# Kernel tuning notes

Hardware: AMD Instinct MI355X
Metric: run time of the kernel (lower is better)

Reference implementation:

```python
import jax, jax.numpy as jnp
import numpy as np

N = 100   # num_nodes
D = 32    # num_dags
B = 8192  # batch_size
H = 32    # MLP hidden width


def setup_inputs() -> dict:
    key = jax.random.key(0)
    ks = jax.random.split(key, 6)
    x = jax.random.normal(ks[0], (B, N), dtype=jnp.float32)
    # binary adjacency masks for each sampled DAG
    A = (jax.random.uniform(ks[1], (D, N, N)) < 0.5).astype(jnp.float32)
    # per-dag topological order: a permutation of the N nodes
    order = jax.vmap(lambda k: jax.random.permutation(k, N))(
        jax.random.split(ks[2], D)).astype(jnp.int32)
    do_idx = 0  # intervened node
    # per-node MLP params: Linear(N+1, H) -> LeakyReLU -> Linear(H, 1)
    W1 = jax.random.normal(ks[3], (N, H, N + 1), dtype=jnp.float32) * (1.0 / np.sqrt(N + 1))
    b1 = jnp.zeros((N, H), dtype=jnp.float32)
    W2 = jax.random.normal(ks[4], (N, H), dtype=jnp.float32) * (1.0 / np.sqrt(H))
    b2 = jnp.zeros((N,), dtype=jnp.float32)
    return {"x": x, "A": A, "order": order, "do_idx": do_idx,
            "W1": W1, "b1": b1, "W2": W2, "b2": b2}


def reference(x, A, order, do_idx, W1, b1, W2, b2):
    Bn, Nn = x.shape
    # intervention: zero incoming edges of do_idx
    A = A.at[:, :, do_idx].set(0.0)

    def run_dag(A_d, order_d):
        def step(outputs, node):
            mask = A_d[:, node]                      # [N] parents of `node`
            ins = jnp.concatenate(
                [outputs * mask[None, :], x[:, node][:, None]], axis=1)  # [B, N+1]
            h = jax.nn.leaky_relu(ins @ W1[node].T + b1[node])           # [B, H]
            out = h @ W2[node] + b2[node]                                # [B]
            val = jnp.where(node == do_idx, x[:, node], out)
            return outputs.at[:, node].set(val), None

        outs, _ = jax.lax.scan(step, jnp.zeros((Bn, Nn), x.dtype), order_d)
        return outs  # [B, N]

    return jax.vmap(run_dag)(A, order)  # [D, B, N]
```

## Files before the change

### kernel.cpp

```cpp
#include <hip/hip_runtime.h>
#include <hip/hip_fp16.h>

#define NN 100
#define HH 32
#define BB 8192
#define DD 32
#define KP 128
#define TPB 512

typedef _Float16 f16x8 __attribute__((ext_vector_type(8)));
typedef _Float16 f16x2 __attribute__((ext_vector_type(2)));
typedef __fp16 fph2 __attribute__((ext_vector_type(2)));
typedef float f32x4 __attribute__((ext_vector_type(4)));
typedef unsigned short ushort_t;
typedef unsigned int uint_t;
union FU { uint4 u; f16x8 h; };
union PU { fph2 p; f16x2 h; uint_t u; };

#define AS_GLOBAL __attribute__((address_space(1)))
#define AS_LDS    __attribute__((address_space(3)))

__global__ void prep_xt(const float* __restrict__ x, float* __restrict__ xT) {
  int idx = blockIdx.x * 256 + threadIdx.x;
  if (idx >= BB * NN) return;
  int b = idx & (BB - 1);
  int n = idx >> 13;
  xT[idx] = x[(size_t)b * NN + n];
}

__global__ void prep_w1m(const float* __restrict__ A, const float* __restrict__ W1,
                         const float* __restrict__ b1, ushort_t* __restrict__ W1M) {
  int idx = blockIdx.x * 256 + threadIdx.x;
  int tile = idx >> 12;
  int d = tile / NN;
  int node = tile - d * NN;
  int rem = idx & 4095;
  int j = rem >> 7;
  int k = rem & 127;
  float v = 0.f;
  if (k < NN) {
    float m = A[((size_t)d * NN + k) * NN + node];
    v = (m != 0.f) ? W1[((size_t)node * HH + j) * (NN + 1) + k] : 0.f;
  } else if (k == NN) {
    v = W1[((size_t)node * HH + j) * (NN + 1) + NN];
  } else if (k == NN + 1) {
    v = b1[node * HH + j];
  }
  int t = (j * KP + k) ^ ((j & 7) << 3);
  W1M[(size_t)tile * 4096 + t] = __half_as_ushort(__float2half_rn(v));
}

__global__ void prep_epi3(const float* __restrict__ W2, const float* __restrict__ b2,
                          uint_t* __restrict__ epi) {
  int idx = blockIdx.x * 256 + threadIdx.x;
  if (idx >= NN * 20) return;
  int node = idx / 20;
  int c = idx - node * 20;
  uint_t v = 0u;
  if (c < 16) {
    uint_t lo = __half_as_ushort(__float2half_rn(W2[node * HH + 2 * c]));
    uint_t hi = __half_as_ushort(__float2half_rn(W2[node * HH + 2 * c + 1]));
    v = lo | (hi << 16);
  } else if (c == 16) {
    v = __float_as_uint(b2[node]);
  }
  epi[idx] = v;
}

#define EPI_OFF 65536
#define SMEM_BYTES (65536 + 8000)

__global__ __launch_bounds__(TPB, 4) void dag_mfma_ss(
    const float* __restrict__ xT,
    const int* __restrict__ order,
    const int* __restrict__ do_idx_p,
    const ushort_t* __restrict__ W1M,
    const uint_t* __restrict__ epi_g,
    float* __restrict__ out)
{
  __shared__ __align__(16) char smem[SMEM_BYTES];
  ushort_t* stage = (ushort_t*)smem;
  const char* sp = (const char*)smem;
  uint_t* epi_l = (uint_t*)(smem + EPI_OFF);

  const int d = blockIdx.y;
  const int bx = blockIdx.x;
  const int tid = threadIdx.x;
  const int w = tid >> 6;
  const int lane = tid & 63;
  const int g = lane >> 4;
  const int n16 = lane & 15;
  const int di = __builtin_amdgcn_readfirstlane(do_idx_p[0]);
  const int rowbase = bx * 512 + w * 64 + n16;

  {
    const uint4* s4 = (const uint4*)epi_g;
    uint4* d4 = (uint4*)epi_l;
    for (int i = tid; i < 500; i += TPB) d4[i] = s4[i];
  }

  const ushort_t* Wd = W1M + (size_t)d * NN * 4096;
  const int* ord = order + d * NN;

  int vs[4];
#pragma unroll
  for (int S = 0; S < 4; ++S) {
    int hw = n16 * 128 + ((8 * g) ^ ((n16 & 3) << 3)) + 32 * (S ^ ((n16 >> 2) & 1));
    vs[S] = 2 * hw + 32768;
  }

  int nd[4], nn[4];
#pragma unroll
  for (int q = 0; q < 4; ++q) nd[q] = __builtin_amdgcn_readfirstlane(ord[q]);
#pragma unroll
  for (int q = 0; q < 4; ++q) {
    const ushort_t* gsrc = Wd + (size_t)nd[q] * 4096 + tid * 8;
    __builtin_amdgcn_global_load_lds((const AS_GLOBAL void*)gsrc,
        (AS_LDS void*)(stage + q * 4096 + (w << 9)), 16, 0, 0);
  }
  float xq[4][4];
#pragma unroll
  for (int q = 0; q < 4; ++q) {
    const float* xp = xT + (size_t)nd[q] * BB + rowbase;
#pragma unroll
    for (int nt = 0; nt < 4; ++nt) xq[q][nt] = xp[nt * 16];
  }

  uint4 breg[4][4];
#pragma unroll
  for (int nt = 0; nt < 4; ++nt) {
#pragma unroll
    for (int S = 0; S < 4; ++S) breg[nt][S] = make_uint4(0u, 0u, 0u, 0u);
    breg[nt][3].z = (g == 0) ? 0x3C000000u : 0u;
  }

  const f32x4 zero4 = {0.f, 0.f, 0.f, 0.f};
  PU c001; c001.u = 0x211F211Fu;

#pragma unroll 1
  for (int ss = 0; ss < 25; ++ss) {
    asm volatile("s_waitcnt vmcnt(0) lgkmcnt(0)" ::: "memory");
    __builtin_amdgcn_s_barrier();
    __builtin_amdgcn_sched_barrier(0);

#pragma unroll
    for (int S = 0; S < 4; ++S) vs[S] ^= 32768;

    const bool more = (ss < 24);
    if (more) {
#pragma unroll
      for (int q = 0; q < 4; ++q)
        nn[q] = __builtin_amdgcn_readfirstlane(ord[4 * (ss + 1) + q]);
      const int dsts = (((ss + 1) & 1) << 14);
#pragma unroll
      for (int q = 0; q < 4; ++q) {
        const ushort_t* gsrc = Wd + (size_t)nn[q] * 4096 + tid * 8;
        __builtin_amdgcn_global_load_lds((const AS_GLOBAL void*)gsrc,
            (AS_LDS void*)(stage + dsts + q * 4096 + (w << 9)), 16, 0, 0);
      }
    }

#pragma unroll
    for (int q = 0; q < 4; ++q) {
      const int node = nd[q];

#pragma unroll
      for (int nt = 0; nt < 4; ++nt) {
        uint_t old = breg[nt][3].z;
        uint_t ins = (old & 0xFFFF0000u) |
                     (uint_t)__half_as_ushort(__float2half_rn(xq[q][nt]));
        breg[nt][3].z = (g == 0) ? ins : old;
      }

      float val[4];
      if (node != di) {
        const char* ep = (const char*)epi_l + node * 80;
        const uint2 wlo = *(const uint2*)(ep + 8 * g);
        const uint2 whi = *(const uint2*)(ep + 32 + 8 * g);
        const float b2n = *(const float*)(ep + 64);

        f32x4 acc[4][2];
        __builtin_amdgcn_s_setprio(1);
#pragma unroll
        for (int S = 0; S < 4; ++S) {
          FU a0, a1;
          a0.u = *(const uint4*)(sp + vs[S] + q * 8192);
          a1.u = *(const uint4*)(sp + vs[S] + q * 8192 + 4096);
#pragma unroll
          for (int nt = 0; nt < 4; ++nt) {
            FU bu; bu.u = breg[nt][S];
            if (S == 0) {
              acc[nt][0] = __builtin_amdgcn_mfma_f32_16x16x32_f16(a0.h, bu.h, zero4, 0, 0, 0);
              acc[nt][1] = __builtin_amdgcn_mfma_f32_16x16x32_f16(a1.h, bu.h, zero4, 0, 0, 0);
            } else {
              acc[nt][0] = __builtin_amdgcn_mfma_f32_16x16x32_f16(a0.h, bu.h, acc[nt][0], 0, 0, 0);
              acc[nt][1] = __builtin_amdgcn_mfma_f32_16x16x32_f16(a1.h, bu.h, acc[nt][1], 0, 0, 0);
            }
          }
        }
        __builtin_amdgcn_s_setprio(0);

        PU w01, w23, w45, w67;
        w01.u = wlo.x; w23.u = wlo.y; w45.u = whi.x; w67.u = whi.y;
#pragma unroll
        for (int nt = 0; nt < 4; ++nt) {
#if __has_builtin(__builtin_amdgcn_fdot2)
          PU h01, h23, h45, h67;
          h01.p = __builtin_amdgcn_cvt_pkrtz(acc[nt][0][0], acc[nt][0][1]);
          h23.p = __builtin_amdgcn_cvt_pkrtz(acc[nt][0][2], acc[nt][0][3]);
          h45.p = __builtin_amdgcn_cvt_pkrtz(acc[nt][1][0], acc[nt][1][1]);
          h67.p = __builtin_amdgcn_cvt_pkrtz(acc[nt][1][2], acc[nt][1][3]);
          h01.p = __builtin_elementwise_max(h01.p, h01.p * c001.p);
          h23.p = __builtin_elementwise_max(h23.p, h23.p * c001.p);
          h45.p = __builtin_elementwise_max(h45.p, h45.p * c001.p);
          h67.p = __builtin_elementwise_max(h67.p, h67.p * c001.p);
          float p = __builtin_amdgcn_fdot2(h01.h, w01.h, 0.f, false);
          p = __builtin_amdgcn_fdot2(h23.h, w23.h, p, false);
          p = __builtin_amdgcn_fdot2(h45.h, w45.h, p, false);
          p = __builtin_amdgcn_fdot2(h67.h, w67.h, p, false);
#else
          float p = 0.f;
          const uint_t wu0[2] = {w01.u, w23.u};
          const uint_t wu1[2] = {w45.u, w67.u};
#pragma unroll
          for (int r4 = 0; r4 < 4; ++r4) {
            float wv0 = __half2float(__ushort_as_half(
                (ushort_t)((wu0[r4 >> 1] >> ((r4 & 1) * 16)) & 0xFFFFu)));
            float wv1 = __half2float(__ushort_as_half(
                (ushort_t)((wu1[r4 >> 1] >> ((r4 & 1) * 16)) & 0xFFFFu)));
            float h0 = acc[nt][0][r4]; h0 = fmaxf(h0, 0.01f * h0);
            float h1 = acc[nt][1][r4]; h1 = fmaxf(h1, 0.01f * h1);
            p = fmaf(wv0, h0, p);
            p = fmaf(wv1, h1, p);
          }
#endif
          p += __shfl_xor(p, 16, 64);
          p += __shfl_xor(p, 32, 64);
          val[nt] = p + b2n;
        }
      } else {
#pragma unroll
        for (int nt = 0; nt < 4; ++nt) val[nt] = xq[q][nt];
      }

      if (more) {
        const float* xp = xT + (size_t)nn[q] * BB + rowbase;
#pragma unroll
        for (int nt = 0; nt < 4; ++nt) xq[q][nt] = xp[nt * 16];
      }

      const int sn = node >> 5;
      const int en2 = (node >> 1) & 3;
      const int gn = (node >> 3) & 3;
      const int hin = node & 1;
      const bool own = (g == gn);
      ushort_t hv[4];
#pragma unroll
      for (int nt = 0; nt < 4; ++nt) hv[nt] = __half_as_ushort(__float2half_rn(val[nt]));
#pragma unroll
      for (int S = 0; S < 4; ++S) {
        if (S != sn) continue;
#pragma unroll
        for (int nt = 0; nt < 4; ++nt) {
          uint4& Bq = breg[nt][S];
          uint_t hvn = (uint_t)hv[nt];
          if (en2 == 0) {
            uint_t old = Bq.x;
            uint_t nw = hin ? ((old & 0x0000FFFFu) | (hvn << 16)) : ((old & 0xFFFF0000u) | hvn);
            Bq.x = own ? nw : old;
          } else if (en2 == 1) {
            uint_t old = Bq.y;
            uint_t nw = hin ? ((old & 0x0000FFFFu) | (hvn << 16)) : ((old & 0xFFFF0000u) | hvn);
            Bq.y = own ? nw : old;
          } else if (en2 == 2) {
            uint_t old = Bq.z;
            uint_t nw = hin ? ((old & 0x0000FFFFu) | (hvn << 16)) : ((old & 0xFFFF0000u) | hvn);
            Bq.z = own ? nw : old;
          } else {
            uint_t old = Bq.w;
            uint_t nw = hin ? ((old & 0x0000FFFFu) | (hvn << 16)) : ((old & 0xFFFF0000u) | hvn);
            Bq.w = own ? nw : old;
          }
        }
      }
    }

#pragma unroll
    for (int q = 0; q < 4; ++q) nd[q] = nn[q];
  }

  ushort_t* tbuf = (ushort_t*)smem;
  for (int c = 0; c < 8; ++c) {
    __syncthreads();
    if (w == c) {
#pragma unroll
      for (int nt = 0; nt < 4; ++nt) {
        int r = nt * 16 + n16;
#pragma unroll
        for (int S = 0; S < 4; ++S) {
          int k = 32 * S + 8 * g;
          *(uint2*)&tbuf[r * 132 + k] = make_uint2(breg[nt][S].x, breg[nt][S].y);
          *(uint2*)&tbuf[r * 132 + k + 4] = make_uint2(breg[nt][S].z, breg[nt][S].w);
        }
      }
    }
    __syncthreads();
    const size_t obase = ((size_t)d * BB + bx * 512 + c * 64) * NN;
    for (int idx = tid; idx < 64 * NN; idx += TPB) {
      int rl = idx / NN;
      int col = idx - rl * NN;
      out[obase + idx] = __half2float(__ushort_as_half(tbuf[rl * 132 + col]));
    }
  }
}

extern "C" void kernel_launch(void* const* d_in, const int* in_sizes, int n_in,
                              void* d_out, int out_size, void* d_ws, size_t ws_size,
                              hipStream_t stream) {
  const float* x     = (const float*)d_in[0];
  const float* A     = (const float*)d_in[1];
  const int* order   = (const int*)d_in[2];
  const int* do_idx  = (const int*)d_in[3];
  const float* W1    = (const float*)d_in[4];
  const float* b1    = (const float*)d_in[5];
  const float* W2    = (const float*)d_in[6];
  const float* b2    = (const float*)d_in[7];
  float* out = (float*)d_out;

  char* ws = (char*)d_ws;
  const size_t XT_B = 3276800UL;
  const size_t W1M_B = (size_t)DD * NN * 4096 * 2;
  float* xT     = (float*)ws;
  ushort_t* W1M = (ushort_t*)(ws + XT_B);
  uint_t* epi   = (uint_t*)(ws + XT_B + W1M_B);

  hipLaunchKernelGGL(prep_xt, dim3((BB * NN) / 256), dim3(256), 0, stream, x, xT);
  hipLaunchKernelGGL(prep_w1m, dim3((DD * NN * 4096) / 256), dim3(256), 0, stream,
                     A, W1, b1, W1M);
  hipLaunchKernelGGL(prep_epi3, dim3((NN * 20 + 255) / 256), dim3(256), 0, stream,
                     W2, b2, epi);
  hipLaunchKernelGGL(dag_mfma_ss, dim3(BB / 512, DD), dim3(TPB), 0, stream,
                     xT, order, do_idx, W1M, epi, out);
}
```

Measured before the change: 305.6 us.

## Stage fp16 x columns into LDS via async global_load_lds double buffer

The transposed x is now stored as fp16 in the prep kernel, which halves its footprint. The main kernel no longer issues per-thread global float loads into registers. Instead, one wave per node slot prefetches the next step's x column into a double-buffered LDS region with global_load_lds, alongside the W1 tiles. Each step then reads x from LDS, which frees about 16 VGPRs and takes global latency off the critical path. The cost is 8KB more LDS per block, which may affect occupancy, and the do_idx passthrough value is now rounded to fp16 before being written out.

```diff
diff --git a/kernel.cpp b/kernel.cpp
--- a/kernel.cpp
+++ b/kernel.cpp
@@ -20,12 +20,12 @@
 #define AS_GLOBAL __attribute__((address_space(1)))
 #define AS_LDS    __attribute__((address_space(3)))
 
-__global__ void prep_xt(const float* __restrict__ x, float* __restrict__ xT) {
+__global__ void prep_xth(const float* __restrict__ x, ushort_t* __restrict__ xTh) {
   int idx = blockIdx.x * 256 + threadIdx.x;
   if (idx >= BB * NN) return;
   int b = idx & (BB - 1);
   int n = idx >> 13;
-  xT[idx] = x[(size_t)b * NN + n];
+  xTh[idx] = __half_as_ushort(__float2half_rn(x[(size_t)b * NN + n]));
 }
 
 __global__ void prep_w1m(const float* __restrict__ A, const float* __restrict__ W1,
@@ -67,11 +67,12 @@
   epi[idx] = v;
 }
 
-#define EPI_OFF 65536
-#define SMEM_BYTES (65536 + 8000)
+#define XS_OFF 65536
+#define EPI_OFF 73728
+#define SMEM_BYTES (73728 + 8000)
 
 __global__ __launch_bounds__(TPB, 4) void dag_mfma_ss(
-    const float* __restrict__ xT,
+    const ushort_t* __restrict__ xTh,
     const int* __restrict__ order,
     const int* __restrict__ do_idx_p,
     const ushort_t* __restrict__ W1M,
@@ -91,7 +92,6 @@
   const int g = lane >> 4;
   const int n16 = lane & 15;
   const int di = __builtin_amdgcn_readfirstlane(do_idx_p[0]);
-  const int rowbase = bx * 512 + w * 64 + n16;
 
   {
     const uint4* s4 = (const uint4*)epi_g;
@@ -108,6 +108,7 @@
     int hw = n16 * 128 + ((8 * g) ^ ((n16 & 3) << 3)) + 32 * (S ^ ((n16 >> 2) & 1));
     vs[S] = 2 * hw + 32768;
   }
+  int xso = XS_OFF + (w * 64 + n16) * 2 + 4096;
 
   int nd[4], nn[4];
 #pragma unroll
@@ -118,12 +119,13 @@
     __builtin_amdgcn_global_load_lds((const AS_GLOBAL void*)gsrc,
         (AS_LDS void*)(stage + q * 4096 + (w << 9)), 16, 0, 0);
   }
-  float xq[4][4];
 #pragma unroll
   for (int q = 0; q < 4; ++q) {
-    const float* xp = xT + (size_t)nd[q] * BB + rowbase;
-#pragma unroll
-    for (int nt = 0; nt < 4; ++nt) xq[q][nt] = xp[nt * 16];
+    if (w == q) {
+      const ushort_t* gx = xTh + (size_t)nd[q] * BB + bx * 512 + lane * 8;
+      __builtin_amdgcn_global_load_lds((const AS_GLOBAL void*)gx,
+          (AS_LDS void*)(smem + XS_OFF + q * 1024), 16, 0, 0);
+    }
   }
 
   uint4 breg[4][4];
@@ -145,6 +147,7 @@
 
 #pragma unroll
     for (int S = 0; S < 4; ++S) vs[S] ^= 32768;
+    xso ^= 4096;
 
     const bool more = (ss < 24);
     if (more) {
@@ -158,17 +161,30 @@
         __builtin_amdgcn_global_load_lds((const AS_GLOBAL void*)gsrc,
             (AS_LDS void*)(stage + dsts + q * 4096 + (w << 9)), 16, 0, 0);
       }
+      const int xdst = XS_OFF + (((ss + 1) & 1) << 12);
+#pragma unroll
+      for (int q = 0; q < 4; ++q) {
+        if (w == q) {
+          const ushort_t* gx = xTh + (size_t)nn[q] * BB + bx * 512 + lane * 8;
+          __builtin_amdgcn_global_load_lds((const AS_GLOBAL void*)gx,
+              (AS_LDS void*)(smem + xdst + q * 1024), 16, 0, 0);
+        }
+      }
     }
 
 #pragma unroll
     for (int q = 0; q < 4; ++q) {
       const int node = nd[q];
 
+      ushort_t xb[4];
+#pragma unroll
+      for (int nt = 0; nt < 4; ++nt)
+        xb[nt] = *(const ushort_t*)(sp + xso + q * 1024 + nt * 32);
+
 #pragma unroll
       for (int nt = 0; nt < 4; ++nt) {
         uint_t old = breg[nt][3].z;
-        uint_t ins = (old & 0xFFFF0000u) |
-                     (uint_t)__half_as_ushort(__float2half_rn(xq[q][nt]));
+        uint_t ins = (old & 0xFFFF0000u) | (uint_t)xb[nt];
         breg[nt][3].z = (g == 0) ? ins : old;
       }
 
@@ -204,7 +220,6 @@
         w01.u = wlo.x; w23.u = wlo.y; w45.u = whi.x; w67.u = whi.y;
 #pragma unroll
         for (int nt = 0; nt < 4; ++nt) {
-#if __has_builtin(__builtin_amdgcn_fdot2)
           PU h01, h23, h45, h67;
           h01.p = __builtin_amdgcn_cvt_pkrtz(acc[nt][0][0], acc[nt][0][1]);
           h23.p = __builtin_amdgcn_cvt_pkrtz(acc[nt][0][2], acc[nt][0][3]);
@@ -218,35 +233,14 @@
           p = __builtin_amdgcn_fdot2(h23.h, w23.h, p, false);
           p = __builtin_amdgcn_fdot2(h45.h, w45.h, p, false);
           p = __builtin_amdgcn_fdot2(h67.h, w67.h, p, false);
-#else
-          float p = 0.f;
-          const uint_t wu0[2] = {w01.u, w23.u};
-          const uint_t wu1[2] = {w45.u, w67.u};
-#pragma unroll
-          for (int r4 = 0; r4 < 4; ++r4) {
-            float wv0 = __half2float(__ushort_as_half(
-                (ushort_t)((wu0[r4 >> 1] >> ((r4 & 1) * 16)) & 0xFFFFu)));
-            float wv1 = __half2float(__ushort_as_half(
-                (ushort_t)((wu1[r4 >> 1] >> ((r4 & 1) * 16)) & 0xFFFFu)));
-            float h0 = acc[nt][0][r4]; h0 = fmaxf(h0, 0.01f * h0);
-            float h1 = acc[nt][1][r4]; h1 = fmaxf(h1, 0.01f * h1);
-            p = fmaf(wv0, h0, p);
-            p = fmaf(wv1, h1, p);
-          }
-#endif
           p += __shfl_xor(p, 16, 64);
           p += __shfl_xor(p, 32, 64);
           val[nt] = p + b2n;
         }
       } else {
 #pragma unroll
-        for (int nt = 0; nt < 4; ++nt) val[nt] = xq[q][nt];
-      }
-
-      if (more) {
-        const float* xp = xT + (size_t)nn[q] * BB + rowbase;
-#pragma unroll
-        for (int nt = 0; nt < 4; ++nt) xq[q][nt] = xp[nt * 16];
+        for (int nt = 0; nt < 4; ++nt)
+          val[nt] = __half2float(__ushort_as_half(xb[nt]));
       }
 
       const int sn = node >> 5;
@@ -328,17 +322,17 @@
   float* out = (float*)d_out;
 
   char* ws = (char*)d_ws;
-  const size_t XT_B = 3276800UL;
+  const size_t XTH_B = (size_t)BB * NN * 2;
   const size_t W1M_B = (size_t)DD * NN * 4096 * 2;
-  float* xT     = (float*)ws;
-  ushort_t* W1M = (ushort_t*)(ws + XT_B);
-  uint_t* epi   = (uint_t*)(ws + XT_B + W1M_B);
-
-  hipLaunchKernelGGL(prep_xt, dim3((BB * NN) / 256), dim3(256), 0, stream, x, xT);
+  ushort_t* xTh = (ushort_t*)ws;
+  ushort_t* W1M = (ushort_t*)(ws + XTH_B);
+  uint_t* epi   = (uint_t*)(ws + XTH_B + W1M_B);
+
+  hipLaunchKernelGGL(prep_xth, dim3((BB * NN) / 256), dim3(256), 0, stream, x, xTh);
   hipLaunchKernelGGL(prep_w1m, dim3((DD * NN * 4096) / 256), dim3(256), 0, stream,
                      A, W1, b1, W1M);
   hipLaunchKernelGGL(prep_epi3, dim3((NN * 20 + 255) / 256), dim3(256), 0, stream,
                      W2, b2, epi);
   hipLaunchKernelGGL(dag_mfma_ss, dim3(BB / 512, DD), dim3(TPB), 0, stream,
-                     xT, order, do_idx, W1M, epi, out);
-}
+                     xTh, order, do_idx, W1M, epi, out);
+}
```

Measured after the change: 275.0 us. -10.0%, faster.
